# Performance work log

Measured on AMD Instinct MI355X. Metric: run time of the kernel, lower is better.

The kernel has to match this reference:

```python
import jax, jax.numpy as jnp
import numpy as np

B = 65536; D1 = 64; D2 = 64; DC = 128; K = 8; DFF = 1024
NPP = 3 * K - 1                      # 23 params per output dim (non-adaptive)
MIN_BIN = 0.1; MIN_DERIV = 1e-3; ALPHA = 2.0
DEFAULT = 3.0; DL = -DEFAULT; DD = 2 * DEFAULT; MIN_DELTA = MIN_BIN * K
SHIFT = float(np.log(np.e - 1.0))
SHIFT_DX = float(np.log(np.exp(DD - MIN_DELTA) - 1.0))
EPS = 1e-6


def setup_inputs() -> dict:
    key = jax.random.key(0)
    ks = jax.random.split(key, 8)
    x1 = jax.random.normal(ks[0], (B, D1), dtype=jnp.float32)
    x2 = jax.random.normal(ks[1], (B, D2), dtype=jnp.float32)
    context = jax.random.normal(ks[2], (B, DC), dtype=jnp.float32)
    mask1 = jnp.ones((B, D1), dtype=jnp.float32)
    din = 2 * D1 + DC
    W0 = jax.random.normal(ks[3], (din, DFF), dtype=jnp.float32) / np.sqrt(din)
    b0 = jnp.zeros((DFF,), jnp.float32)
    W1 = jax.random.normal(ks[4], (DFF, DFF), dtype=jnp.float32) / np.sqrt(DFF)
    b1 = jnp.zeros((DFF,), jnp.float32)
    W2 = jax.random.normal(ks[5], (DFF, DFF), dtype=jnp.float32) / np.sqrt(DFF)
    b2 = jnp.zeros((DFF,), jnp.float32)
    W3 = jax.random.normal(ks[6], (DFF, NPP * D2), dtype=jnp.float32) / np.sqrt(DFF)
    b3 = jnp.zeros((NPP * D2,), jnp.float32)
    return dict(x1=x1, x2=x2, context=context, mask1=mask1,
                W0=W0, b0=b0, W1=W1, b1=b1, W2=W2, b2=b2, W3=W3, b3=b3)


def _rq_forward(x1, x2, context, mask1, W0, b0, W1, b1, W2, b2, W3, b3):
    # --- conditioner MLP: input = concat(x1, mask1, context) ---
    h = jnp.concatenate([x1, mask1, context], axis=-1)
    h = jax.nn.relu(h @ W0 + b0)
    h = jax.nn.relu(h @ W1 + b1)
    h = jax.nn.relu(h @ W2 + b2)
    params = (h @ W3 + b3).reshape(x1.shape[0], D2, NPP)  # [B, D2, 23]

    w_raw = params[..., :K]
    h_raw = params[..., K:2 * K]
    d_raw = params[..., 2 * K:3 * K - 1]
    zeros = jnp.zeros(params.shape[:-1] + (1,), params.dtype)  # non-adaptive raw params

    # --- _constrain ---
    log_weight = ALPHA * jnp.tanh(zeros / ALPHA)          # -> 0
    weight = jnp.exp(log_weight)                          # -> 1
    bias = ALPHA * jnp.tanh(zeros / ALPHA)                # -> 0
    derivs = MIN_DERIV + jax.nn.softplus(d_raw + SHIFT)
    derivs = jnp.concatenate([weight, derivs, weight], axis=-1)  # [B, D2, K+1]
    left = DL + DD * jnp.tanh(zeros / DD)                 # -> -3
    delta_x = MIN_DELTA + jax.nn.softplus(zeros + SHIFT_DX)
    right = left + delta_x                                # -> +3
    bottom = weight * left + bias
    top = weight * right + bias

    w = jax.nn.softmax(w_raw, axis=-1)
    w = MIN_BIN + (1.0 - MIN_BIN * K) * w
    cw = jnp.pad(jnp.cumsum(w, axis=-1), ((0, 0), (0, 0), (1, 0)))
    cw = (right - left) * cw + left                       # cumwidths [B, D2, K+1]
    hh = jax.nn.softmax(h_raw, axis=-1)
    hh = MIN_BIN + (1.0 - MIN_BIN * K) * hh
    ch = jnp.pad(jnp.cumsum(hh, axis=-1), ((0, 0), (0, 0), (1, 0)))
    ch = (top - bottom) * ch + bottom                     # cumheights [B, D2, K+1]

    widths = cw[..., 1:] - cw[..., :-1]
    heights = ch[..., 1:] - ch[..., :-1]

    # --- bin search (searchsorted right=True on bumped cumwidths) ---
    bumped = jnp.concatenate([cw[..., :-1], cw[..., -1:] + EPS], axis=-1)
    idx = jnp.clip(jnp.sum(bumped <= x2[..., None], axis=-1) - 1, 0, K - 1)[..., None]

    gat = lambda t: jnp.take_along_axis(t, idx, axis=-1)[..., 0]
    x_k = gat(cw); x_kd = gat(widths)
    y_k = gat(ch); y_kd = gat(heights)
    s_k = gat(heights / widths)
    d0 = gat(derivs); d1 = gat(derivs[..., 1:])

    # --- forward rational-quadratic spline ---
    xi = (x2 - x_k) / x_kd
    xi1m = xi * (1.0 - xi)
    alpha_k = y_kd * (s_k * xi ** 2 + d0 * xi1m)
    beta_k = s_k + (d1 + d0 - 2.0 * s_k) * xi1m
    z_sp = y_k + alpha_k / jnp.maximum(beta_k, 1e-8)
    num = s_k ** 2 * (d1 * xi ** 2 + 2.0 * s_k * xi1m + d0 * (1.0 - xi) ** 2)
    ld_sp = jnp.log(jnp.maximum(num, 1e-8)) - 2.0 * jnp.log(jnp.maximum(beta_k, 1e-8))

    # --- affine tails ---
    lw = log_weight[..., 0]; bs = bias[..., 0]
    z_af = jnp.exp(lw) * x2 + bs
    ld_af = jnp.broadcast_to(lw, x2.shape)

    l2 = jnp.broadcast_to(left[..., 0], x2.shape)
    r2 = jnp.broadcast_to(right[..., 0], x2.shape)
    inside = (l2 <= x2) & (x2 < r2)
    z2 = jnp.where(inside, z_sp, z_af)
    ld = jnp.where(inside, ld_sp, ld_af)
    return z2, ld.sum(-1)


def reference(x1, x2, context, mask1, W0, b0, W1, b1, W2, b2, W3, b3):
    return _rq_forward(x1, x2, context, mask1, W0, b0, W1, b1, W2, b2, W3, b3)
```

## Files before the change

### kernel.cpp

```cpp
#include <hip/hip_runtime.h>


typedef __bf16 bf16_t;
typedef __bf16 bf16x8 __attribute__((ext_vector_type(8)));
typedef float f32x4 __attribute__((ext_vector_type(4)));

#define GLOAD_LDS16(g, l)                                               \
  __builtin_amdgcn_global_load_lds(                                     \
      (const __attribute__((address_space(1))) void*)(g),               \
      (__attribute__((address_space(3))) void*)(l), 16, 0, 0)

__global__ __launch_bounds__(256) void transpose_w(
    const float* __restrict__ W, bf16_t* __restrict__ Wt,
    int K, int N, int Npad) {
  __shared__ float tile[64][65];
  const int kt = blockIdx.x * 64;
  const int nt = blockIdx.y * 64;
  const int r4 = threadIdx.x >> 6;
  const int c = threadIdx.x & 63;
#pragma unroll
  for (int i = 0; i < 16; i++) {
    int r = i * 4 + r4;
    int gn = nt + c;
    tile[r][c] = (gn < N) ? W[(size_t)(kt + r) * N + gn] : 0.0f;
  }
  __syncthreads();
#pragma unroll
  for (int i = 0; i < 16; i++) {
    int r = i * 4 + r4;
    Wt[(size_t)(nt + r) * K + kt + c] = (bf16_t)tile[c][r];
  }
}

__global__ __launch_bounds__(256) void transpose_w3p(
    const float* __restrict__ W3, bf16_t* __restrict__ Wt) {
  __shared__ float tile[64][65];
  const int kt = blockIdx.x * 64;
  const int nt = blockIdx.y * 64;
  const int r4 = threadIdx.x >> 6;
  const int c = threadIdx.x & 63;
  const int np = nt + c;
  const int d = np / 24, p = np % 24;
#pragma unroll
  for (int i = 0; i < 16; i++) {
    int r = i * 4 + r4;
    tile[r][c] = (p < 23) ? W3[(size_t)(kt + r) * 1472 + d * 23 + p] : 0.0f;
  }
  __syncthreads();
#pragma unroll
  for (int i = 0; i < 16; i++) {
    int r = i * 4 + r4;
    Wt[(size_t)(nt + r) * 1024 + kt + c] = (bf16_t)tile[c][r];
  }
}

__global__ __launch_bounds__(256) void prep_b3(const float* __restrict__ b3,
                                               float* __restrict__ b3p) {
  int t = blockIdx.x * 256 + threadIdx.x;
  if (t < 1536) {
    int d = t / 24, p = t % 24;
    b3p[t] = (p < 23) ? b3[d * 23 + p] : 0.0f;
  }
}

__global__ __launch_bounds__(256) void build_x(
    const float* __restrict__ x1, const float* __restrict__ mask1,
    const float* __restrict__ ctx, bf16_t* __restrict__ X,
    float* __restrict__ ld_out, int boff) {
  int idx = blockIdx.x * 256 + threadIdx.x;
  int bl = idx >> 8;
  int c = idx & 255;
  size_t b = (size_t)(boff + bl);
  float v;
  if (c < 64)       v = x1[b * 64 + c];
  else if (c < 128) v = mask1[b * 64 + (c - 64)];
  else              v = ctx[b * 128 + (c - 128)];
  X[(size_t)bl * 256 + c] = (bf16_t)v;
  if (c == 0) ld_out[b] = 0.0f;
}

__global__ __launch_bounds__(512, 4) void gemm_bt(
    const bf16_t* __restrict__ A, const bf16_t* __restrict__ Bt,
    const float* __restrict__ bias, bf16_t* __restrict__ Cout, int N, int K) {
  __shared__ __align__(16) bf16_t As[2][128 * 32];
  __shared__ __align__(16) bf16_t Bs[2][256 * 32];
  const int tid = threadIdx.x;
  const int w = tid >> 6;
  const int lane = tid & 63;
  const int m0 = blockIdx.y * 128;
  const int n0 = blockIdx.x * 256;
  const int wm = (w & 1) * 64;
  const int wn = (w >> 1) * 64;
  const int lrow = lane & 15;
  const int quad = lane >> 4;

  const bf16_t* gA;
  {
    const int byteoff = (w << 10) + lane * 16;
    const int row = byteoff >> 6;
    const int qs = ((byteoff >> 4) & 3) ^ ((row >> 1) & 3);
    gA = A + (size_t)(m0 + row) * K + qs * 8;
  }
  const bf16_t* gB0;
  const bf16_t* gB1;
  {
    int byteoff = (w << 10) + lane * 16;
    int row = byteoff >> 6;
    int qs = ((byteoff >> 4) & 3) ^ ((row >> 1) & 3);
    gB0 = Bt + (size_t)(n0 + row) * K + qs * 8;
    byteoff = ((w + 8) << 10) + lane * 16;
    row = byteoff >> 6;
    qs = ((byteoff >> 4) & 3) ^ ((row >> 1) & 3);
    gB1 = Bt + (size_t)(n0 + row) * K + qs * 8;
  }
  bf16_t* const dA0 = &As[0][0] + w * 512;
  bf16_t* const dB0 = &Bs[0][0] + w * 512;
  bf16_t* const dB1 = &Bs[0][0] + (w + 8) * 512;

  int offA[4], offB[4];
#pragma unroll
  for (int i = 0; i < 4; i++) {
    const int rowA = wm + i * 16 + lrow;
    offA[i] = rowA * 32 + (quad ^ ((rowA >> 1) & 3)) * 8;
    const int rowB = wn + i * 16 + lrow;
    offB[i] = rowB * 32 + (quad ^ ((rowB >> 1) & 3)) * 8;
  }

  f32x4 acc[4][4];
#pragma unroll
  for (int i = 0; i < 4; i++)
#pragma unroll
    for (int j = 0; j < 4; j++) acc[i][j] = (f32x4){0.f, 0.f, 0.f, 0.f};

  const int nPair = K >> 6;
  for (int kp = 0; kp < nPair; kp++) {
    GLOAD_LDS16(gA, dA0);
    GLOAD_LDS16(gA + 32, dA0 + 4096);
    GLOAD_LDS16(gB0, dB0);
    GLOAD_LDS16(gB0 + 32, dB0 + 8192);
    GLOAD_LDS16(gB1, dB1);
    GLOAD_LDS16(gB1 + 32, dB1 + 8192);
    gA += 64;
    gB0 += 64;
    gB1 += 64;
    __syncthreads();
#pragma unroll
    for (int h = 0; h < 2; h++) {
      bf16x8 af[4], bfr[4];
#pragma unroll
      for (int i = 0; i < 4; i++)
        af[i] = *(const bf16x8*)(&As[0][0] + h * 4096 + offA[i]);
#pragma unroll
      for (int j = 0; j < 4; j++)
        bfr[j] = *(const bf16x8*)(&Bs[0][0] + h * 8192 + offB[j]);
#pragma unroll
      for (int i = 0; i < 4; i++)
#pragma unroll
        for (int j = 0; j < 4; j++)
          acc[i][j] = __builtin_amdgcn_mfma_f32_16x16x32_bf16(
              af[i], bfr[j], acc[i][j], 0, 0, 0);
    }
    __syncthreads();
  }

  float bv[4];
#pragma unroll
  for (int j = 0; j < 4; j++) bv[j] = bias[n0 + wn + j * 16 + lrow];
#pragma unroll
  for (int i = 0; i < 4; i++) {
    int rbase = m0 + wm + i * 16 + quad * 4;
#pragma unroll
    for (int j = 0; j < 4; j++) {
      int col = n0 + wn + j * 16 + lrow;
#pragma unroll
      for (int r = 0; r < 4; r++) {
        float v = fmaxf(acc[i][j][r] + bv[j], 0.0f);
        Cout[(size_t)(rbase + r) * N + col] = (bf16_t)v;
      }
    }
  }
}

__global__ __launch_bounds__(512, 4) void gemm_rq_fused(
    const bf16_t* __restrict__ A, const bf16_t* __restrict__ Bt,
    const float* __restrict__ b3p, const float* __restrict__ x2,
    float* __restrict__ z_out, float* __restrict__ ld_out,
    int boff, int K) {
  union alignas(16) SM {
    struct { bf16_t As[2][128 * 32]; bf16_t Bs[2][192 * 32]; } s;
    bf16_t Pt[128 * 200];
  };
  __shared__ SM sm;
  const int tid = threadIdx.x;
  const int w = tid >> 6;
  const int lane = tid & 63;
  const int m0 = blockIdx.y * 128;
  const int n0 = blockIdx.x * 192;
  const int wm = (w & 1) * 64;
  const int wn = (w >> 1) * 48;
  const int lrow = lane & 15;
  const int quad = lane >> 4;

  bf16_t* const smB = &sm.s.As[0][0];

  const bf16_t* gA;
  {
    const int byteoff = (w << 10) + lane * 16;
    const int row = byteoff >> 6;
    const int qs = ((byteoff >> 4) & 3) ^ ((row >> 1) & 3);
    gA = A + (size_t)(m0 + row) * K + qs * 8;
  }
  const bf16_t* gB0;
  const bf16_t* gB1;
  {
    int byteoff = (w << 10) + lane * 16;
    int row = byteoff >> 6;
    int qs = ((byteoff >> 4) & 3) ^ ((row >> 1) & 3);
    gB0 = Bt + (size_t)(n0 + row) * K + qs * 8;
    const int c1 = (w & 3) + 8;
    byteoff = (c1 << 10) + lane * 16;
    row = byteoff >> 6;
    qs = ((byteoff >> 4) & 3) ^ ((row >> 1) & 3);
    gB1 = Bt + (size_t)(n0 + row) * K + qs * 8;
  }
  bf16_t* const dA0 = smB + w * 512;
  bf16_t* const dB0 = smB + 8192 + w * 512;
  bf16_t* const dB1 = smB + 8192 + ((w & 3) + 8) * 512;

  int offA[4], offB3[3];
#pragma unroll
  for (int i = 0; i < 4; i++) {
    const int rowA = wm + i * 16 + lrow;
    offA[i] = rowA * 32 + (quad ^ ((rowA >> 1) & 3)) * 8;
  }
#pragma unroll
  for (int j = 0; j < 3; j++) {
    const int rowB = wn + j * 16 + lrow;
    offB3[j] = rowB * 32 + (quad ^ ((rowB >> 1) & 3)) * 8;
  }

  f32x4 acc[4][3];
#pragma unroll
  for (int i = 0; i < 4; i++)
#pragma unroll
    for (int j = 0; j < 3; j++) acc[i][j] = (f32x4){0.f, 0.f, 0.f, 0.f};

  const int nPair = K >> 6;
  for (int kp = 0; kp < nPair; kp++) {
    GLOAD_LDS16(gA, dA0);
    GLOAD_LDS16(gA + 32, dA0 + 4096);
    GLOAD_LDS16(gB0, dB0);
    GLOAD_LDS16(gB0 + 32, dB0 + 6144);
    if (w < 4) {
      GLOAD_LDS16(gB1, dB1);
      GLOAD_LDS16(gB1 + 32, dB1 + 6144);
      gB1 += 64;
    }
    gA += 64;
    gB0 += 64;
    __syncthreads();
#pragma unroll
    for (int h = 0; h < 2; h++) {
      bf16x8 af[4], bfr[3];
#pragma unroll
      for (int i = 0; i < 4; i++)
        af[i] = *(const bf16x8*)(smB + h * 4096 + offA[i]);
#pragma unroll
      for (int j = 0; j < 3; j++)
        bfr[j] = *(const bf16x8*)(smB + 8192 + h * 6144 + offB3[j]);
#pragma unroll
      for (int i = 0; i < 4; i++)
#pragma unroll
        for (int j = 0; j < 3; j++)
          acc[i][j] = __builtin_amdgcn_mfma_f32_16x16x32_bf16(
              af[i], bfr[j], acc[i][j], 0, 0, 0);
    }
    __syncthreads();
  }

  float bv[3];
#pragma unroll
  for (int j = 0; j < 3; j++) bv[j] = b3p[n0 + wn + j * 16 + lrow];
#pragma unroll
  for (int i = 0; i < 4; i++) {
    const int rbase = wm + i * 16 + quad * 4;
#pragma unroll
    for (int j = 0; j < 3; j++) {
      const int col = wn + j * 16 + lrow;
#pragma unroll
      for (int r = 0; r < 4; r++)
        sm.Pt[(rbase + r) * 200 + col] = (bf16_t)(acc[i][j][r] + bv[j]);
    }
  }
  __syncthreads();

  const float SHIFT = 0.54132485f;
  const float SHIFT_DX = 5.1944682f;
  const float left = -3.0f;
  const float delta_x = 0.8f + log1pf(expf(SHIFT_DX));
  const float right = left + delta_x;
  const float scale = delta_x;
  const int dloc = tid & 7;
  const int dg = blockIdx.x * 8 + dloc;

#pragma unroll
  for (int rr = 0; rr < 2; rr++) {
    const int row = (tid >> 3) + rr * 64;
    const bf16_t* pr = sm.Pt + row * 200 + dloc * 24;
    const size_t bg = (size_t)(boff + m0 + row);
    const float x = x2[bg * 64 + dg];

    bf16x8 v0 = *(const bf16x8*)(pr);
    bf16x8 v1 = *(const bf16x8*)(pr + 8);
    bf16x8 v2 = *(const bf16x8*)(pr + 16);
    float pv[24];
#pragma unroll
    for (int j = 0; j < 8; j++) pv[j] = (float)v0[j];
#pragma unroll
    for (int j = 0; j < 8; j++) pv[8 + j] = (float)v1[j];
#pragma unroll
    for (int j = 0; j < 8; j++) pv[16 + j] = (float)v2[j];

    float mw = pv[0];
#pragma unroll
    for (int j = 1; j < 8; j++) mw = fmaxf(mw, pv[j]);
    float ew[8], swv = 0.f;
#pragma unroll
    for (int j = 0; j < 8; j++) { ew[j] = expf(pv[j] - mw); swv += ew[j]; }
    float invw = 1.0f / swv;
    float cw[9];
    cw[0] = left;
    float cum = 0.f;
#pragma unroll
    for (int j = 0; j < 8; j++) {
      cum += 0.1f + 0.2f * ew[j] * invw;
      cw[j + 1] = left + scale * cum;
    }
    float mh = pv[8];
#pragma unroll
    for (int j = 9; j < 16; j++) mh = fmaxf(mh, pv[j]);
    float eh[8], shv = 0.f;
#pragma unroll
    for (int j = 0; j < 8; j++) { eh[j] = expf(pv[8 + j] - mh); shv += eh[j]; }
    float invh = 1.0f / shv;
    float chh[9];
    chh[0] = left;
    float cumh = 0.f;
#pragma unroll
    for (int j = 0; j < 8; j++) {
      cumh += 0.1f + 0.2f * eh[j] * invh;
      chh[j + 1] = left + scale * cumh;
    }
    float dv[9];
    dv[0] = 1.0f;
    dv[8] = 1.0f;
#pragma unroll
    for (int j = 0; j < 7; j++) {
      float v = pv[16 + j] + SHIFT;
      dv[j + 1] = 0.001f + ((v > 20.f) ? v : log1pf(expf(v)));
    }
    int cnt = 0;
#pragma unroll
    for (int j = 0; j < 8; j++) cnt += (cw[j] <= x) ? 1 : 0;
    cnt += ((cw[8] + 1e-6f) <= x) ? 1 : 0;
    int idx = cnt - 1;
    idx = idx < 0 ? 0 : (idx > 7 ? 7 : idx);
    float x_k = cw[0], x_k1 = cw[1], y_k = chh[0], y_k1 = chh[1];
    float d0v = dv[0], d1v = dv[1];
#pragma unroll
    for (int j = 1; j < 8; j++) {
      bool s = (idx == j);
      x_k = s ? cw[j] : x_k;
      x_k1 = s ? cw[j + 1] : x_k1;
      y_k = s ? chh[j] : y_k;
      y_k1 = s ? chh[j + 1] : y_k1;
      d0v = s ? dv[j] : d0v;
      d1v = s ? dv[j + 1] : d1v;
    }
    float x_kd = x_k1 - x_k;
    float y_kd = y_k1 - y_k;
    float s_k = y_kd / x_kd;
    float xi = (x - x_k) / x_kd;
    float xi1m = xi * (1.f - xi);
    float alpha_k = y_kd * (s_k * xi * xi + d0v * xi1m);
    float beta_k = s_k + (d1v + d0v - 2.f * s_k) * xi1m;
    float z_sp = y_k + alpha_k / fmaxf(beta_k, 1e-8f);
    float oxi = 1.f - xi;
    float num = s_k * s_k * (d1v * xi * xi + 2.f * s_k * xi1m + d0v * oxi * oxi);
    float ld_sp = logf(fmaxf(num, 1e-8f)) - 2.f * logf(fmaxf(beta_k, 1e-8f));

    bool inside = (left <= x) && (x < right);
    z_out[bg * 64 + dg] = inside ? z_sp : x;
    float ldv = inside ? ld_sp : 0.f;
    ldv += __shfl_xor(ldv, 1);
    ldv += __shfl_xor(ldv, 2);
    ldv += __shfl_xor(ldv, 4);
    if (dloc == 0) atomicAdd(&ld_out[bg], ldv);
  }
}

extern "C" void kernel_launch(void* const* d_in, const int* in_sizes, int n_in,
                              void* d_out, int out_size, void* d_ws,
                              size_t ws_size, hipStream_t stream) {
  const float* x1 = (const float*)d_in[0];
  const float* x2 = (const float*)d_in[1];
  const float* ctx = (const float*)d_in[2];
  const float* mask1 = (const float*)d_in[3];
  const float* W0 = (const float*)d_in[4];
  const float* b0 = (const float*)d_in[5];
  const float* W1 = (const float*)d_in[6];
  const float* b1 = (const float*)d_in[7];
  const float* W2 = (const float*)d_in[8];
  const float* b2 = (const float*)d_in[9];
  const float* W3 = (const float*)d_in[10];
  const float* b3 = (const float*)d_in[11];
  float* out = (float*)d_out;

  const int B = 65536;
  char* ws = (char*)d_ws;

  bf16_t* Wt0 = (bf16_t*)ws;
  bf16_t* Wt1 = (bf16_t*)(ws + 524288);
  bf16_t* Wt2 = (bf16_t*)(ws + 524288 + 2097152);
  bf16_t* Wt3 = (bf16_t*)(ws + 524288 + 2 * 2097152);
  float* b3p = (float*)(ws + 524288 + 2 * 2097152 + 3145728);
  const size_t wend = 524288 + 2 * 2097152 + 3145728 + 8192;

  int C = 4;
  if (wend + (size_t)B * 4096 <= ws_size) C = 1;
  else if (wend + (size_t)(B / 2) * 4096 <= ws_size) C = 2;
  const int Bc = B / C;
  bf16_t* HA = (bf16_t*)(ws + wend);
  char* R = ws + wend + (size_t)Bc * 2048;
  bf16_t* X = (bf16_t*)R;
  bf16_t* HB = (bf16_t*)R;
  float* ld_out = out + (size_t)B * 64;

  transpose_w<<<dim3(4, 16), 256, 0, stream>>>(W0, Wt0, 256, 1024, 1024);
  transpose_w<<<dim3(16, 16), 256, 0, stream>>>(W1, Wt1, 1024, 1024, 1024);
  transpose_w<<<dim3(16, 16), 256, 0, stream>>>(W2, Wt2, 1024, 1024, 1024);
  transpose_w3p<<<dim3(16, 24), 256, 0, stream>>>(W3, Wt3);
  prep_b3<<<6, 256, 0, stream>>>(b3, b3p);

  for (int c = 0; c < C; c++) {
    const int boff = c * Bc;
    build_x<<<Bc, 256, 0, stream>>>(x1, mask1, ctx, X, ld_out, boff);
    gemm_bt<<<dim3(4, Bc / 128), 512, 0, stream>>>(X, Wt0, b0, HA, 1024, 256);
    gemm_bt<<<dim3(4, Bc / 128), 512, 0, stream>>>(HA, Wt1, b1, HB, 1024, 1024);
    gemm_bt<<<dim3(4, Bc / 128), 512, 0, stream>>>(HB, Wt2, b2, HA, 1024, 1024);
    gemm_rq_fused<<<dim3(8, Bc / 128), 512, 0, stream>>>(
        HA, Wt3, b3p, x2, out, ld_out, boff, 1024);
  }
}
```

Before: 819.2 us.

## Double-buffer LDS k-tiles with async global-to-LDS prefetch in both GEMMs

The two MFMA GEMM main loops now stage K=32 slices into alternating LDS halves. The next slice is issued with global_load_lds right after the current fragments are read into registers, so the global loads overlap the MFMA work instead of sitting behind a barrier. A sched_barrier and s_setprio around the MFMA block add scheduling hints. The change halves the work per barrier and relies on a single barrier per step to guard against buffer reuse races.

Measured after the change: 892.7 us. 1.09x slower.

```diff
diff --git a/kernel.cpp b/kernel.cpp
--- a/kernel.cpp
+++ b/kernel.cpp
@@ -113,9 +113,6 @@
     qs = ((byteoff >> 4) & 3) ^ ((row >> 1) & 3);
     gB1 = Bt + (size_t)(n0 + row) * K + qs * 8;
   }
-  bf16_t* const dA0 = &As[0][0] + w * 512;
-  bf16_t* const dB0 = &Bs[0][0] + w * 512;
-  bf16_t* const dB1 = &Bs[0][0] + (w + 8) * 512;
 
   int offA[4], offB[4];
 #pragma unroll
@@ -132,36 +129,45 @@
 #pragma unroll
     for (int j = 0; j < 4; j++) acc[i][j] = (f32x4){0.f, 0.f, 0.f, 0.f};
 
-  const int nPair = K >> 6;
-  for (int kp = 0; kp < nPair; kp++) {
-    GLOAD_LDS16(gA, dA0);
-    GLOAD_LDS16(gA + 32, dA0 + 4096);
-    GLOAD_LDS16(gB0, dB0);
-    GLOAD_LDS16(gB0 + 32, dB0 + 8192);
-    GLOAD_LDS16(gB1, dB1);
-    GLOAD_LDS16(gB1 + 32, dB1 + 8192);
-    gA += 64;
-    gB0 += 64;
-    gB1 += 64;
+#define MID_STAGE(NXT)                                                  \
+  {                                                                     \
+    GLOAD_LDS16(gA, &As[NXT][0] + w * 512);                             \
+    GLOAD_LDS16(gB0, &Bs[NXT][0] + w * 512);                            \
+    GLOAD_LDS16(gB1, &Bs[NXT][0] + (w + 8) * 512);                      \
+    gA += 32; gB0 += 32; gB1 += 32;                                     \
+  }
+
+#define MID_STEP(CUR, NXT, DO_STAGE)                                    \
+  {                                                                     \
+    bf16x8 af[4], bfr[4];                                               \
+    _Pragma("unroll") for (int i = 0; i < 4; i++)                       \
+      af[i] = *(const bf16x8*)(&As[CUR][0] + offA[i]);                  \
+    _Pragma("unroll") for (int j = 0; j < 4; j++)                       \
+      bfr[j] = *(const bf16x8*)(&Bs[CUR][0] + offB[j]);                 \
+    if (DO_STAGE) MID_STAGE(NXT);                                       \
+    __builtin_amdgcn_sched_barrier(0);                                  \
+    __builtin_amdgcn_s_setprio(1);                                      \
+    _Pragma("unroll") for (int i = 0; i < 4; i++)                       \
+      _Pragma("unroll") for (int j = 0; j < 4; j++)                     \
+        acc[i][j] = __builtin_amdgcn_mfma_f32_16x16x32_bf16(            \
+            af[i], bfr[j], acc[i][j], 0, 0, 0);                         \
+    __builtin_amdgcn_s_setprio(0);                                      \
+  }
+
+  const int nt = K >> 5;
+  MID_STAGE(0);
+  __syncthreads();
+  for (int t = 0; t < nt - 2; t += 2) {
+    MID_STEP(0, 1, 1);
     __syncthreads();
-#pragma unroll
-    for (int h = 0; h < 2; h++) {
-      bf16x8 af[4], bfr[4];
-#pragma unroll
-      for (int i = 0; i < 4; i++)
-        af[i] = *(const bf16x8*)(&As[0][0] + h * 4096 + offA[i]);
-#pragma unroll
-      for (int j = 0; j < 4; j++)
-        bfr[j] = *(const bf16x8*)(&Bs[0][0] + h * 8192 + offB[j]);
-#pragma unroll
-      for (int i = 0; i < 4; i++)
-#pragma unroll
-        for (int j = 0; j < 4; j++)
-          acc[i][j] = __builtin_amdgcn_mfma_f32_16x16x32_bf16(
-              af[i], bfr[j], acc[i][j], 0, 0, 0);
-    }
+    MID_STEP(1, 0, 1);
     __syncthreads();
   }
+  MID_STEP(0, 1, 1);
+  __syncthreads();
+  MID_STEP(1, 0, 0);
+#undef MID_STAGE
+#undef MID_STEP
 
   float bv[4];
 #pragma unroll
@@ -223,9 +229,6 @@
     qs = ((byteoff >> 4) & 3) ^ ((row >> 1) & 3);
     gB1 = Bt + (size_t)(n0 + row) * K + qs * 8;
   }
-  bf16_t* const dA0 = smB + w * 512;
-  bf16_t* const dB0 = smB + 8192 + w * 512;
-  bf16_t* const dB1 = smB + 8192 + ((w & 3) + 8) * 512;
 
   int offA[4], offB3[3];
 #pragma unroll
@@ -245,38 +248,49 @@
 #pragma unroll
     for (int j = 0; j < 3; j++) acc[i][j] = (f32x4){0.f, 0.f, 0.f, 0.f};
 
-  const int nPair = K >> 6;
-  for (int kp = 0; kp < nPair; kp++) {
-    GLOAD_LDS16(gA, dA0);
-    GLOAD_LDS16(gA + 32, dA0 + 4096);
-    GLOAD_LDS16(gB0, dB0);
-    GLOAD_LDS16(gB0 + 32, dB0 + 6144);
-    if (w < 4) {
-      GLOAD_LDS16(gB1, dB1);
-      GLOAD_LDS16(gB1 + 32, dB1 + 6144);
-      gB1 += 64;
-    }
-    gA += 64;
-    gB0 += 64;
+#define FUS_STAGE(NXT)                                                  \
+  {                                                                     \
+    GLOAD_LDS16(gA, smB + (NXT) * 4096 + w * 512);                      \
+    GLOAD_LDS16(gB0, smB + 8192 + (NXT) * 6144 + w * 512);              \
+    gA += 32; gB0 += 32;                                                \
+    if (w < 4) {                                                        \
+      GLOAD_LDS16(gB1, smB + 8192 + (NXT) * 6144 + ((w & 3) + 8) * 512);\
+      gB1 += 32;                                                        \
+    }                                                                   \
+  }
+
+#define FUS_STEP(CUR, NXT, DO_STAGE)                                    \
+  {                                                                     \
+    bf16x8 af[4], bfr[3];                                               \
+    _Pragma("unroll") for (int i = 0; i < 4; i++)                       \
+      af[i] = *(const bf16x8*)(smB + (CUR) * 4096 + offA[i]);           \
+    _Pragma("unroll") for (int j = 0; j < 3; j++)                       \
+      bfr[j] = *(const bf16x8*)(smB + 8192 + (CUR) * 6144 + offB3[j]);  \
+    if (DO_STAGE) FUS_STAGE(NXT);                                       \
+    __builtin_amdgcn_sched_barrier(0);                                  \
+    __builtin_amdgcn_s_setprio(1);                                      \
+    _Pragma("unroll") for (int i = 0; i < 4; i++)                       \
+      _Pragma("unroll") for (int j = 0; j < 3; j++)                     \
+        acc[i][j] = __builtin_amdgcn_mfma_f32_16x16x32_bf16(            \
+            af[i], bfr[j], acc[i][j], 0, 0, 0);                         \
+    __builtin_amdgcn_s_setprio(0);                                      \
+  }
+
+  const int nt = K >> 5;
+  FUS_STAGE(0);
+  __syncthreads();
+  for (int t = 0; t < nt - 2; t += 2) {
+    FUS_STEP(0, 1, 1);
     __syncthreads();
-#pragma unroll
-    for (int h = 0; h < 2; h++) {
-      bf16x8 af[4], bfr[3];
-#pragma unroll
-      for (int i = 0; i < 4; i++)
-        af[i] = *(const bf16x8*)(smB + h * 4096 + offA[i]);
-#pragma unroll
-      for (int j = 0; j < 3; j++)
-        bfr[j] = *(const bf16x8*)(smB + 8192 + h * 6144 + offB3[j]);
-#pragma unroll
-      for (int i = 0; i < 4; i++)
-#pragma unroll
-        for (int j = 0; j < 3; j++)
-          acc[i][j] = __builtin_amdgcn_mfma_f32_16x16x32_bf16(
-              af[i], bfr[j], acc[i][j], 0, 0, 0);
-    }
+    FUS_STEP(1, 0, 1);
     __syncthreads();
   }
+  FUS_STEP(0, 1, 1);
+  __syncthreads();
+  FUS_STEP(1, 0, 0);
+#undef FUS_STAGE
+#undef FUS_STEP
+  __syncthreads();
 
   float bv[3];
 #pragma unroll
```

## Double-buffer LDS tiles with async prefetch in MLP and fused spline GEMMs

Applied to the files above, without the earlier changes.

Replaces the load-then-compute K loop in both GEMM kernels with a two-stage ring over 32-wide K slices. The next slice's global-to-LDS loads are issued after the fragments are read into registers, and explicit vmcnt/lgkmcnt waits plus raw barriers replace __syncthreads. The goal is to hide global memory latency behind the MFMA work instead of stalling each iteration. In exchange, each K step is half as deep, so there are more barriers per unit of work. The hand-counted waitcnt values are fragile and depend on the per-wave load count (3 or 2).

After: 864.2 us. 5.5% more time.

```diff
diff --git a/kernel.cpp b/kernel.cpp
--- a/kernel.cpp
+++ b/kernel.cpp
@@ -9,6 +9,11 @@
   __builtin_amdgcn_global_load_lds(                                     \
       (const __attribute__((address_space(1))) void*)(g),               \
       (__attribute__((address_space(3))) void*)(l), 16, 0, 0)
+
+#define WAITVM(N) asm volatile("s_waitcnt vmcnt(" #N ")" ::: "memory")
+#define WAITLGKM0 asm volatile("s_waitcnt lgkmcnt(0)" ::: "memory")
+#define SBAR() __builtin_amdgcn_s_barrier()
+#define SCHEDB() __builtin_amdgcn_sched_barrier(0)
 
 __global__ __launch_bounds__(256) void transpose_w(
     const float* __restrict__ W, bf16_t* __restrict__ Wt,
@@ -113,9 +118,6 @@
     qs = ((byteoff >> 4) & 3) ^ ((row >> 1) & 3);
     gB1 = Bt + (size_t)(n0 + row) * K + qs * 8;
   }
-  bf16_t* const dA0 = &As[0][0] + w * 512;
-  bf16_t* const dB0 = &Bs[0][0] + w * 512;
-  bf16_t* const dB1 = &Bs[0][0] + (w + 8) * 512;
 
   int offA[4], offB[4];
 #pragma unroll
@@ -132,36 +134,41 @@
 #pragma unroll
     for (int j = 0; j < 4; j++) acc[i][j] = (f32x4){0.f, 0.f, 0.f, 0.f};
 
-  const int nPair = K >> 6;
-  for (int kp = 0; kp < nPair; kp++) {
-    GLOAD_LDS16(gA, dA0);
-    GLOAD_LDS16(gA + 32, dA0 + 4096);
-    GLOAD_LDS16(gB0, dB0);
-    GLOAD_LDS16(gB0 + 32, dB0 + 8192);
-    GLOAD_LDS16(gB1, dB1);
-    GLOAD_LDS16(gB1 + 32, dB1 + 8192);
-    gA += 64;
-    gB0 += 64;
-    gB1 += 64;
-    __syncthreads();
-#pragma unroll
-    for (int h = 0; h < 2; h++) {
-      bf16x8 af[4], bfr[4];
-#pragma unroll
-      for (int i = 0; i < 4; i++)
-        af[i] = *(const bf16x8*)(&As[0][0] + h * 4096 + offA[i]);
+#define MID_STAGE(BUF)                                                  \
+  do {                                                                  \
+    GLOAD_LDS16(gA, &As[BUF][0] + w * 512);                             \
+    GLOAD_LDS16(gB0, &Bs[BUF][0] + w * 512);                            \
+    GLOAD_LDS16(gB1, &Bs[BUF][0] + (w + 8) * 512);                      \
+    gA += 32; gB0 += 32; gB1 += 32;                                     \
+  } while (0)
+
+  const int nt = K >> 5;
+  MID_STAGE(0);
+  MID_STAGE(1);
+  for (int t = 0; t < nt; t++) {
+    const int cur = t & 1;
+    if (t + 1 < nt) WAITVM(3); else WAITVM(0);
+    SBAR();
+    SCHEDB();
+    bf16x8 af[4], bfr[4];
+#pragma unroll
+    for (int i = 0; i < 4; i++)
+      af[i] = *(const bf16x8*)(&As[cur][0] + offA[i]);
+#pragma unroll
+    for (int j = 0; j < 4; j++)
+      bfr[j] = *(const bf16x8*)(&Bs[cur][0] + offB[j]);
+    WAITLGKM0;
+    SBAR();
+    SCHEDB();
+    if (t + 2 < nt) MID_STAGE(cur);
+#pragma unroll
+    for (int i = 0; i < 4; i++)
 #pragma unroll
       for (int j = 0; j < 4; j++)
-        bfr[j] = *(const bf16x8*)(&Bs[0][0] + h * 8192 + offB[j]);
-#pragma unroll
-      for (int i = 0; i < 4; i++)
-#pragma unroll
-        for (int j = 0; j < 4; j++)
-          acc[i][j] = __builtin_amdgcn_mfma_f32_16x16x32_bf16(
-              af[i], bfr[j], acc[i][j], 0, 0, 0);
-    }
-    __syncthreads();
-  }
+        acc[i][j] = __builtin_amdgcn_mfma_f32_16x16x32_bf16(
+            af[i], bfr[j], acc[i][j], 0, 0, 0);
+  }
+#undef MID_STAGE
 
   float bv[4];
 #pragma unroll
@@ -200,6 +207,7 @@
   const int wn = (w >> 1) * 48;
   const int lrow = lane & 15;
   const int quad = lane >> 4;
+  const int wu = __builtin_amdgcn_readfirstlane(w);
 
   bf16_t* const smB = &sm.s.As[0][0];
 
@@ -223,9 +231,6 @@
     qs = ((byteoff >> 4) & 3) ^ ((row >> 1) & 3);
     gB1 = Bt + (size_t)(n0 + row) * K + qs * 8;
   }
-  bf16_t* const dA0 = smB + w * 512;
-  bf16_t* const dB0 = smB + 8192 + w * 512;
-  bf16_t* const dB1 = smB + 8192 + ((w & 3) + 8) * 512;
 
   int offA[4], offB3[3];
 #pragma unroll
@@ -245,38 +250,49 @@
 #pragma unroll
     for (int j = 0; j < 3; j++) acc[i][j] = (f32x4){0.f, 0.f, 0.f, 0.f};
 
-  const int nPair = K >> 6;
-  for (int kp = 0; kp < nPair; kp++) {
-    GLOAD_LDS16(gA, dA0);
-    GLOAD_LDS16(gA + 32, dA0 + 4096);
-    GLOAD_LDS16(gB0, dB0);
-    GLOAD_LDS16(gB0 + 32, dB0 + 6144);
-    if (w < 4) {
-      GLOAD_LDS16(gB1, dB1);
-      GLOAD_LDS16(gB1 + 32, dB1 + 6144);
-      gB1 += 64;
-    }
-    gA += 64;
-    gB0 += 64;
-    __syncthreads();
-#pragma unroll
-    for (int h = 0; h < 2; h++) {
-      bf16x8 af[4], bfr[3];
-#pragma unroll
-      for (int i = 0; i < 4; i++)
-        af[i] = *(const bf16x8*)(smB + h * 4096 + offA[i]);
+#define FUS_STAGE(BUF)                                                  \
+  do {                                                                  \
+    GLOAD_LDS16(gA, smB + (BUF) * 4096 + w * 512);                      \
+    GLOAD_LDS16(gB0, smB + 8192 + (BUF) * 6144 + w * 512);              \
+    gA += 32; gB0 += 32;                                                \
+    if (wu < 4) {                                                       \
+      GLOAD_LDS16(gB1, smB + 8192 + (BUF) * 6144 + ((w & 3) + 8) * 512);\
+      gB1 += 32;                                                        \
+    }                                                                   \
+  } while (0)
+
+  const int nt = K >> 5;
+  FUS_STAGE(0);
+  FUS_STAGE(1);
+  for (int t = 0; t < nt; t++) {
+    const int cur = t & 1;
+    if (t + 1 < nt) {
+      if (wu < 4) WAITVM(3); else WAITVM(2);
+    } else {
+      WAITVM(0);
+    }
+    SBAR();
+    SCHEDB();
+    bf16x8 af[4], bfr[3];
+#pragma unroll
+    for (int i = 0; i < 4; i++)
+      af[i] = *(const bf16x8*)(smB + cur * 4096 + offA[i]);
+#pragma unroll
+    for (int j = 0; j < 3; j++)
+      bfr[j] = *(const bf16x8*)(smB + 8192 + cur * 6144 + offB3[j]);
+    WAITLGKM0;
+    SBAR();
+    SCHEDB();
+    if (t + 2 < nt) FUS_STAGE(cur);
+#pragma unroll
+    for (int i = 0; i < 4; i++)
 #pragma unroll
       for (int j = 0; j < 3; j++)
-        bfr[j] = *(const bf16x8*)(smB + 8192 + h * 6144 + offB3[j]);
-#pragma unroll
-      for (int i = 0; i < 4; i++)
-#pragma unroll
-        for (int j = 0; j < 3; j++)
-          acc[i][j] = __builtin_amdgcn_mfma_f32_16x16x32_bf16(
-              af[i], bfr[j], acc[i][j], 0, 0, 0);
-    }
-    __syncthreads();
-  }
+        acc[i][j] = __builtin_amdgcn_mfma_f32_16x16x32_bf16(
+            af[i], bfr[j], acc[i][j], 0, 0, 0);
+  }
+#undef FUS_STAGE
+  __syncthreads();
 
   float bv[3];
 #pragma unroll
```
